# Kernel optimization log

Hardware: AMD Instinct MI355X
Metric: run time of the kernel (lower is better)

Reference implementation:

```python
import jax, jax.numpy as jnp
import numpy as np

N_NODES = 50000
N_EDGES = 800000
IN_DIM, HID, OUT_DIM = 128, 128, 64
BN_EPS = 1e-5


def setup_inputs() -> dict:
    key = jax.random.key(0)
    ks = jax.random.split(key, 16)
    x = jax.random.normal(ks[0], (N_NODES, IN_DIM), dtype=jnp.float32)
    edge_index = jax.random.randint(ks[1], (2, N_EDGES), 0, N_NODES, dtype=jnp.int64)
    s = 0.05
    params = {
        'Wl1': jax.random.normal(ks[2], (HID, IN_DIM), jnp.float32) * s,
        'Wr1': jax.random.normal(ks[3], (HID, IN_DIM), jnp.float32) * s,
        'b1': jnp.zeros((HID,), jnp.float32),
        'g1': jnp.ones((HID,), jnp.float32),
        'be1': jnp.zeros((HID,), jnp.float32),
        'Wl2': jax.random.normal(ks[4], (HID, HID), jnp.float32) * s,
        'Wr2': jax.random.normal(ks[5], (HID, HID), jnp.float32) * s,
        'b2': jnp.zeros((HID,), jnp.float32),
        'g2': jnp.ones((HID,), jnp.float32),
        'be2': jnp.zeros((HID,), jnp.float32),
        'Wl3': jax.random.normal(ks[6], (OUT_DIM, HID), jnp.float32) * s,
        'Wr3': jax.random.normal(ks[7], (OUT_DIM, HID), jnp.float32) * s,
        'b3': jnp.zeros((OUT_DIM,), jnp.float32),
    }
    return {'x': x, 'edge_index': edge_index, **params}


def _sage_conv(x, src, dst, Wl, Wr, b):
    # PyG SAGEConv (mean): out = lin_l(mean_{j in N(i)} x_j) + lin_r(x_i)
    msg = x[src]  # [E, d] gather
    agg = jax.ops.segment_sum(msg, dst, num_segments=N_NODES)
    cnt = jax.ops.segment_sum(jnp.ones((src.shape[0],), x.dtype), dst, num_segments=N_NODES)
    mean = agg / jnp.maximum(cnt, 1.0)[:, None]
    return mean @ Wl.T + x @ Wr.T + b


def _bn(h, gamma, beta):
    mu = jnp.mean(h, axis=0)
    var = jnp.var(h, axis=0)
    return (h - mu) * jax.lax.rsqrt(var + BN_EPS) * gamma + beta


def reference(x, edge_index, Wl1, Wr1, b1, g1, be1, Wl2, Wr2, b2, g2, be2, Wl3, Wr3, b3):
    src, dst = edge_index[0], edge_index[1]
    h = _sage_conv(x, src, dst, Wl1, Wr1, b1)
    h = jax.nn.relu(_bn(h, g1, be1))
    h = _sage_conv(h, src, dst, Wl2, Wr2, b2)
    h = jax.nn.relu(_bn(h, g2, be2))
    h = _sage_conv(h, src, dst, Wl3, Wr3, b3)
    return h
```

## Files before the change

### kernel.cpp

```cpp
#include <hip/hip_runtime.h>

#define N_NODES 50000
#define N_EDGES 800000
#define BN_EPS 1e-5f
#define NB 196
#define BCAP 5120
#define SCAT_BLOCKS 400
#define EPB 2000
#define GGRID 391

typedef __bf16 bf16x8 __attribute__((ext_vector_type(8)));
typedef float f32x4 __attribute__((ext_vector_type(4)));

static __device__ __forceinline__ unsigned short f2b(float f) {
    unsigned int u = __float_as_uint(f);
    return (unsigned short)((u + 0x7FFFu + ((u >> 16) & 1u)) >> 16);
}
static __device__ __forceinline__ float bl(unsigned int u) { return __uint_as_float(u << 16); }
static __device__ __forceinline__ float bh(unsigned int u) { return __uint_as_float(u & 0xFFFF0000u); }

static __device__ __forceinline__ void gload16(const void* g, void* l) {
    __builtin_amdgcn_global_load_lds(
        (const __attribute__((address_space(1))) unsigned int*)g,
        (__attribute__((address_space(3))) unsigned int*)l, 16, 0, 0);
}

__global__ void init_gcur(int* __restrict__ gcur) {
    int t = threadIdx.x;
    if (t < NB) gcur[t] = t * BCAP;
}

__global__ __launch_bounds__(256) void bucket_scatter(const int* __restrict__ ei,
                                                      int* __restrict__ gcur,
                                                      unsigned int* __restrict__ bdata) {
    __shared__ int hist[NB];
    __shared__ int lcur[NB];
    int t = threadIdx.x;
    if (t < NB) hist[t] = 0;
    __syncthreads();
    int e0 = blockIdx.x * EPB;
    for (int i = t; i < EPB; i += 256) {
        int d = ei[N_EDGES + e0 + i];
        atomicAdd(&hist[d >> 8], 1);
    }
    __syncthreads();
    if (t < NB) lcur[t] = atomicAdd(&gcur[t], hist[t]);
    __syncthreads();
    for (int i = t; i < EPB; i += 256) {
        int d = ei[N_EDGES + e0 + i];
        int s = ei[e0 + i];
        int b = d >> 8;
        int p = atomicAdd(&lcur[b], 1);
        if (p < (b + 1) * BCAP)
            bdata[p] = (unsigned int)s | ((unsigned int)(d & 255) << 16);
    }
}

__global__ __launch_bounds__(256) void scan_buckets(const int* __restrict__ gcur,
                                                    int* __restrict__ bbase,
                                                    int* __restrict__ row) {
    __shared__ int sm[256];
    int t = threadIdx.x;
    int v = 0;
    if (t < NB) {
        v = gcur[t] - t * BCAP;
        if (v > BCAP) v = BCAP;
    }
    sm[t] = v;
    __syncthreads();
    int x = v;
    for (int off = 1; off < 256; off <<= 1) {
        int y = (t >= off) ? sm[t - off] : 0;
        __syncthreads();
        x += y;
        sm[t] = x;
        __syncthreads();
    }
    if (t < NB) bbase[t] = x - v;
    if (t == 0) row[N_NODES] = N_EDGES;
}

__global__ __launch_bounds__(256) void bucket_fill(const unsigned int* __restrict__ bdata,
                                                   const int* __restrict__ gcur,
                                                   const int* __restrict__ bbase,
                                                   int* __restrict__ row,
                                                   int* __restrict__ csrc) {
    __shared__ unsigned int ent[BCAP];
    __shared__ int lcnt[256];
    __shared__ int sm[256];
    __shared__ int cur[256];
    int b = blockIdx.x;
    int t = threadIdx.x;
    int cnt = gcur[b] - b * BCAP;
    if (cnt > BCAP) cnt = BCAP;
    int base = bbase[b];
    for (int i = t; i < cnt; i += 256) ent[i] = bdata[b * BCAP + i];
    lcnt[t] = 0;
    __syncthreads();
    for (int i = t; i < cnt; i += 256) atomicAdd(&lcnt[(ent[i] >> 16) & 255], 1);
    __syncthreads();
    int v = lcnt[t];
    sm[t] = v;
    __syncthreads();
    int x = v;
    for (int off = 1; off < 256; off <<= 1) {
        int y = (t >= off) ? sm[t - off] : 0;
        __syncthreads();
        x += y;
        sm[t] = x;
        __syncthreads();
    }
    int pre = x - v;
    int node = b * 256 + t;
    if (node < N_NODES) row[node] = base + pre;
    cur[t] = base + pre;
    __syncthreads();
    for (int i = t; i < cnt; i += 256) {
        unsigned int e = ent[i];
        int p = atomicAdd(&cur[(e >> 16) & 255], 1);
        csrc[p] = (int)(e & 0xFFFFu);
    }
}

__global__ __launch_bounds__(256) void cast_x(const float* __restrict__ in,
                                              unsigned short* __restrict__ out) {
    int idx = blockIdx.x * 256 + threadIdx.x;
    if (idx >= N_NODES * 32) return;
    float4 v = ((const float4*)in)[idx];
    uint2 p;
    p.x = (unsigned int)f2b(v.x) | ((unsigned int)f2b(v.y) << 16);
    p.y = (unsigned int)f2b(v.z) | ((unsigned int)f2b(v.w) << 16);
    ((uint2*)out)[idx] = p;
}

__global__ void wpack(const float* __restrict__ Wl1, const float* __restrict__ Wr1,
                      const float* __restrict__ Wl2, const float* __restrict__ Wr2,
                      const float* __restrict__ Wl3, const float* __restrict__ Wr3,
                      unsigned short* __restrict__ wp) {
    int idx = blockIdx.x * 256 + threadIdx.x;
    if (idx >= 81920) return;
    const float *Wl, *Wr;
    int rel, base;
    if (idx < 32768)       { Wl = Wl1; Wr = Wr1; rel = idx;         base = 0; }
    else if (idx < 65536)  { Wl = Wl2; Wr = Wr2; rel = idx - 32768; base = 32768; }
    else                   { Wl = Wl3; Wr = Wr3; rel = idx - 65536; base = 65536; }
    int o = rel >> 8;
    int k = rel & 255;
    float v = (k < 128) ? Wl[o * 128 + k] : Wr[o * 128 + (k - 128)];
    int nfAll = o >> 4, lr = o & 15;
    int kc = k >> 5, ko = (k >> 3) & 3, kj = k & 7;
    int lane = ko * 16 + lr;
    wp[base + (((nfAll * 8 + kc) * 64 + lane) << 3) + kj] = f2b(v);
}

template <bool ACT>
__global__ __launch_bounds__(256) void agg_mean_bf16(const unsigned short* __restrict__ xin,
                                                     const int* __restrict__ row,
                                                     const int* __restrict__ csrc,
                                                     const float* __restrict__ scl,
                                                     const float* __restrict__ shf,
                                                     unsigned short* __restrict__ mean) {
    int half = threadIdx.x >> 5;
    int hl = threadIdx.x & 31;
    int node = blockIdx.x * 8 + half;
    if (node >= N_NODES) return;
    float4 sc{}, sh{};
    if (ACT) {
        sc = ((const float4*)scl)[hl];
        sh = ((const float4*)shf)[hl];
    }
    int r0 = row[node], r1 = row[node + 1];
    const uint2* x2 = (const uint2*)xin;
    float a0 = 0.f, a1 = 0.f, a2 = 0.f, a3 = 0.f;
    auto val = [&](float raw, float s, float h) {
        return ACT ? fmaxf(fmaf(raw, s, h), 0.f) : raw;
    };
    int j = r0;
    for (; j + 1 < r1; j += 2) {
        int s0 = csrc[j];
        int s1 = csrc[j + 1];
        uint2 v0 = x2[(size_t)s0 * 32 + hl];
        uint2 v1 = x2[(size_t)s1 * 32 + hl];
        a0 += val(bl(v0.x), sc.x, sh.x) + val(bl(v1.x), sc.x, sh.x);
        a1 += val(bh(v0.x), sc.y, sh.y) + val(bh(v1.x), sc.y, sh.y);
        a2 += val(bl(v0.y), sc.z, sh.z) + val(bl(v1.y), sc.z, sh.z);
        a3 += val(bh(v0.y), sc.w, sh.w) + val(bh(v1.y), sc.w, sh.w);
    }
    if (j < r1) {
        uint2 v = x2[(size_t)csrc[j] * 32 + hl];
        a0 += val(bl(v.x), sc.x, sh.x);
        a1 += val(bh(v.x), sc.y, sh.y);
        a2 += val(bl(v.y), sc.z, sh.z);
        a3 += val(bh(v.y), sc.w, sh.w);
    }
    int deg = r1 - r0;
    float inv = 1.0f / (float)(deg > 1 ? deg : 1);
    uint2 pk;
    pk.x = (unsigned int)f2b(a0 * inv) | ((unsigned int)f2b(a1 * inv) << 16);
    pk.y = (unsigned int)f2b(a2 * inv) | ((unsigned int)f2b(a3 * inv) << 16);
    ((uint2*)mean)[(size_t)node * 32 + hl] = pk;
}

template <int O, bool BF16OUT, bool STATS, bool ACTX>
__global__ __launch_bounds__(256, 1) void gemm_mfma(const unsigned short* __restrict__ Am,
                                                    const unsigned short* __restrict__ Ax,
                                                    const unsigned short* __restrict__ wp,
                                                    const float* __restrict__ bias,
                                                    const float* __restrict__ sclx,
                                                    const float* __restrict__ shfx,
                                                    unsigned short* __restrict__ hout,
                                                    float* __restrict__ fout,
                                                    float* __restrict__ cs,
                                                    float* __restrict__ cq) {
    constexpr int NFW = O / 64;
    __shared__ uint4 abuf[4096];
    char* lds = (char*)abuf;
    int t = threadIdx.x;
    int wv = t >> 6, l = t & 63;
    int lr = l & 15, ko = l >> 4;

    int t0 = blockIdx.x;
    int t1 = t0 + GGRID;

    uint4 wfr[NFW][8];
#pragma unroll
    for (int nf = 0; nf < NFW; ++nf)
#pragma unroll
        for (int kc = 0; kc < 8; ++kc)
            wfr[nf][kc] = *(const uint4*)(wp + (size_t)(((wv * NFW + nf) * 8 + kc) * 512) + l * 8);

    float sacc[NFW], qacc[NFW];
#pragma unroll
    for (int nf = 0; nf < NFW; ++nf) { sacc[nf] = 0.f; qacc[nf] = 0.f; }

    auto STAGE = [&](int buf, int tile) {
        int rbase = tile * 64;
        char* bdst = lds + buf * 32768;
#pragma unroll
        for (int i = 0; i < 8; ++i) {
            int sb = wv * 8 + i;
            int half = sb >> 4;
            int rloc = (sb & 15) * 4 + (l >> 4);
            int grow = rbase + rloc;
            if (grow >= N_NODES) grow = N_NODES - 1;
            int clog = (l & 15) ^ (rloc & 7);
            const unsigned short* src = half ? Ax : Am;
            gload16(src + (size_t)grow * 128 + clog * 8, bdst + sb * 1024);
        }
    };

    auto COMPUTE = [&](int buf, int tile) {
        const char* ab = lds + buf * 32768;
        f32x4 acc[4][NFW];
#pragma unroll
        for (int rt = 0; rt < 4; ++rt)
#pragma unroll
            for (int nf = 0; nf < NFW; ++nf) acc[rt][nf] = (f32x4){0.f, 0.f, 0.f, 0.f};

#pragma unroll
        for (int kc = 0; kc < 8; ++kc) {
            int clog = (kc & 3) * 4 + ko;
            float4 s0{}, s1{}, h0{}, h1{};
            if (ACTX && kc >= 4) {
                int f0 = clog * 8;
                s0 = *(const float4*)(sclx + f0);
                s1 = *(const float4*)(sclx + f0 + 4);
                h0 = *(const float4*)(shfx + f0);
                h1 = *(const float4*)(shfx + f0 + 4);
            }
#pragma unroll
            for (int rt = 0; rt < 4; ++rt) {
                int rloc = rt * 16 + lr;
                int cphys = clog ^ (rloc & 7);
                bf16x8 af = *(const bf16x8*)(ab + (kc >> 2) * 16384 + rloc * 256 + cphys * 16);
                if (ACTX && kc >= 4) {
                    uint4 u = *(uint4*)&af;
                    uint4 r;
                    float e0 = fmaxf(fmaf(bl(u.x), s0.x, h0.x), 0.f);
                    float e1 = fmaxf(fmaf(bh(u.x), s0.y, h0.y), 0.f);
                    float e2 = fmaxf(fmaf(bl(u.y), s0.z, h0.z), 0.f);
                    float e3 = fmaxf(fmaf(bh(u.y), s0.w, h0.w), 0.f);
                    float e4 = fmaxf(fmaf(bl(u.z), s1.x, h1.x), 0.f);
                    float e5 = fmaxf(fmaf(bh(u.z), s1.y, h1.y), 0.f);
                    float e6 = fmaxf(fmaf(bl(u.w), s1.z, h1.z), 0.f);
                    float e7 = fmaxf(fmaf(bh(u.w), s1.w, h1.w), 0.f);
                    r.x = (unsigned int)f2b(e0) | ((unsigned int)f2b(e1) << 16);
                    r.y = (unsigned int)f2b(e2) | ((unsigned int)f2b(e3) << 16);
                    r.z = (unsigned int)f2b(e4) | ((unsigned int)f2b(e5) << 16);
                    r.w = (unsigned int)f2b(e6) | ((unsigned int)f2b(e7) << 16);
                    af = *(bf16x8*)&r;
                }
#pragma unroll
                for (int nf = 0; nf < NFW; ++nf) {
                    bf16x8 wf = *(bf16x8*)&wfr[nf][kc];
                    acc[rt][nf] = __builtin_amdgcn_mfma_f32_16x16x32_bf16(af, wf, acc[rt][nf], 0, 0, 0);
                }
            }
        }

        int rbase = tile * 64;
#pragma unroll
        for (int rt = 0; rt < 4; ++rt) {
            int orow0 = rbase + rt * 16 + ko * 4;
#pragma unroll
            for (int nf = 0; nf < NFW; ++nf) {
                int col = (wv * NFW + nf) * 16 + lr;
                float bs = bias[col];
#pragma unroll
                for (int j = 0; j < 4; ++j) {
                    int r = orow0 + j;
                    if (r < N_NODES) {
                        float v = acc[rt][nf][j] + bs;
                        if (BF16OUT) hout[(size_t)r * 128 + col] = f2b(v);
                        else         fout[(size_t)r * 64 + col] = v;
                        if (STATS) { sacc[nf] += v; qacc[nf] += v * v; }
                    }
                }
            }
        }
    };

    STAGE(0, t0);
    __syncthreads();
    STAGE(1, t1);
    COMPUTE(0, t0);
    __syncthreads();
    COMPUTE(1, t1);

    if (STATS) {
#pragma unroll
        for (int nf = 0; nf < NFW; ++nf) {
            float s = sacc[nf], q = qacc[nf];
            s += __shfl_xor(s, 16);
            s += __shfl_xor(s, 32);
            q += __shfl_xor(q, 16);
            q += __shfl_xor(q, 32);
            if (ko == 0) {
                int col = (wv * NFW + nf) * 16 + lr;
                atomicAdd(&cs[col], s);
                atomicAdd(&cq[col], q);
            }
        }
    }
}

__global__ void bn_prep(const float* __restrict__ cs, const float* __restrict__ cq,
                        const float* __restrict__ g, const float* __restrict__ be,
                        float* __restrict__ scale, float* __restrict__ shift) {
    int f = threadIdx.x;
    float mu = cs[f] * (1.0f / N_NODES);
    float var = cq[f] * (1.0f / N_NODES) - mu * mu;
    float sc = g[f] * rsqrtf(var + BN_EPS);
    scale[f] = sc;
    shift[f] = be[f] - mu * sc;
}

extern "C" void kernel_launch(void* const* d_in, const int* in_sizes, int n_in,
                              void* d_out, int out_size, void* d_ws, size_t ws_size,
                              hipStream_t stream) {
    const float* x   = (const float*)d_in[0];
    const int*   ei  = (const int*)d_in[1];
    const float* Wl1 = (const float*)d_in[2];
    const float* Wr1 = (const float*)d_in[3];
    const float* b1  = (const float*)d_in[4];
    const float* g1  = (const float*)d_in[5];
    const float* be1 = (const float*)d_in[6];
    const float* Wl2 = (const float*)d_in[7];
    const float* Wr2 = (const float*)d_in[8];
    const float* b2  = (const float*)d_in[9];
    const float* g2  = (const float*)d_in[10];
    const float* be2 = (const float*)d_in[11];
    const float* Wl3 = (const float*)d_in[12];
    const float* Wr3 = (const float*)d_in[13];
    const float* b3  = (const float*)d_in[14];
    float* out = (float*)d_out;

    char* p = (char*)d_ws;
    size_t off = 0;
    auto alloc = [&](size_t bytes) {
        char* r = p + off;
        off = (off + bytes + 255) & ~(size_t)255;
        return r;
    };
    int*            gcur  = (int*)alloc((size_t)NB * 4);
    int*            bbase = (int*)alloc((size_t)NB * 4);
    unsigned int*   bdata = (unsigned int*)alloc((size_t)NB * BCAP * 4);
    int*            row   = (int*)alloc((size_t)(N_NODES + 1) * 4);
    int*            csrc  = (int*)alloc((size_t)N_EDGES * 4);
    unsigned short* xb    = (unsigned short*)alloc((size_t)N_NODES * 128 * 2);
    unsigned short* mn    = (unsigned short*)alloc((size_t)N_NODES * 128 * 2);
    unsigned short* h1    = (unsigned short*)alloc((size_t)N_NODES * 128 * 2);
    unsigned short* h2    = (unsigned short*)alloc((size_t)N_NODES * 128 * 2);
    unsigned short* wpb   = (unsigned short*)alloc((size_t)81920 * 2);
    float*          cs    = (float*)alloc(256 * 4);
    float*          cq    = cs + 128;
    float*          scl1  = (float*)alloc(128 * 4);
    float*          shf1  = (float*)alloc(128 * 4);
    float*          scl2  = (float*)alloc(128 * 4);
    float*          shf2  = (float*)alloc(128 * 4);
    (void)ws_size; (void)n_in; (void)in_sizes; (void)out_size;

    unsigned short* wp1 = wpb;
    unsigned short* wp2 = wpb + 32768;
    unsigned short* wp3 = wpb + 65536;

    const int NBLK8 = (N_NODES + 7) / 8;
    const int CBLK  = (N_NODES * 32 + 255) / 256;

    cast_x<<<CBLK, 256, 0, stream>>>(x, xb);
    wpack<<<320, 256, 0, stream>>>(Wl1, Wr1, Wl2, Wr2, Wl3, Wr3, wpb);
    init_gcur<<<1, 256, 0, stream>>>(gcur);
    bucket_scatter<<<SCAT_BLOCKS, 256, 0, stream>>>(ei, gcur, bdata);
    scan_buckets<<<1, 256, 0, stream>>>(gcur, bbase, row);
    bucket_fill<<<NB, 256, 0, stream>>>(bdata, gcur, bbase, row, csrc);

    agg_mean_bf16<false><<<NBLK8, 256, 0, stream>>>(xb, row, csrc, nullptr, nullptr, mn);
    hipMemsetAsync(cs, 0, 256 * 4, stream);
    gemm_mfma<128, true, true, false><<<GGRID, 256, 0, stream>>>(
        mn, xb, wp1, b1, nullptr, nullptr, h1, nullptr, cs, cq);
    bn_prep<<<1, 128, 0, stream>>>(cs, cq, g1, be1, scl1, shf1);

    agg_mean_bf16<true><<<NBLK8, 256, 0, stream>>>(h1, row, csrc, scl1, shf1, mn);
    hipMemsetAsync(cs, 0, 256 * 4, stream);
    gemm_mfma<128, true, true, true><<<GGRID, 256, 0, stream>>>(
        mn, h1, wp2, b2, scl1, shf1, h2, nullptr, cs, cq);
    bn_prep<<<1, 128, 0, stream>>>(cs, cq, g2, be2, scl2, shf2);

    agg_mean_bf16<true><<<NBLK8, 256, 0, stream>>>(h2, row, csrc, scl2, shf2, mn);
    gemm_mfma<64, false, false, true><<<GGRID, 256, 0, stream>>>(
        mn, h2, wp3, b3, scl2, shf2, nullptr, out, nullptr, nullptr);
}
```

Baseline: 229.1 us.

## Shrink GEMM tiles to 32 rows per block and raise occupancy

The node-feature GEMM now processes one 32-row tile per block over 1563 blocks, instead of two 64-row tiles per block over 391 blocks with one block per CU. It drops the occupancy-1 launch bound and cuts LDS from 64 KB to 16 KB so several blocks can share a CU and hide load latency. It also widens the XOR swizzle to 16 and starts the tile load before the weight-fragment load. In exchange, each block reloads its weight fragments into registers, so weight traffic roughly quadruples. The number of BN-statistics atomics per column also rises with the block count.

```diff
diff --git a/kernel.cpp b/kernel.cpp
--- a/kernel.cpp
+++ b/kernel.cpp
@@ -7,7 +7,7 @@
 #define BCAP 5120
 #define SCAT_BLOCKS 400
 #define EPB 2000
-#define GGRID 391
+#define GRB 1563
 
 typedef __bf16 bf16x8 __attribute__((ext_vector_type(8)));
 typedef float f32x4 __attribute__((ext_vector_type(4)));
@@ -202,25 +202,35 @@
 }
 
 template <int O, bool BF16OUT, bool STATS, bool ACTX>
-__global__ __launch_bounds__(256, 1) void gemm_mfma(const unsigned short* __restrict__ Am,
-                                                    const unsigned short* __restrict__ Ax,
-                                                    const unsigned short* __restrict__ wp,
-                                                    const float* __restrict__ bias,
-                                                    const float* __restrict__ sclx,
-                                                    const float* __restrict__ shfx,
-                                                    unsigned short* __restrict__ hout,
-                                                    float* __restrict__ fout,
-                                                    float* __restrict__ cs,
-                                                    float* __restrict__ cq) {
+__global__ __launch_bounds__(256) void gemm_mfma(const unsigned short* __restrict__ Am,
+                                                 const unsigned short* __restrict__ Ax,
+                                                 const unsigned short* __restrict__ wp,
+                                                 const float* __restrict__ bias,
+                                                 const float* __restrict__ sclx,
+                                                 const float* __restrict__ shfx,
+                                                 unsigned short* __restrict__ hout,
+                                                 float* __restrict__ fout,
+                                                 float* __restrict__ cs,
+                                                 float* __restrict__ cq) {
     constexpr int NFW = O / 64;
-    __shared__ uint4 abuf[4096];
+    __shared__ uint4 abuf[1024];
     char* lds = (char*)abuf;
     int t = threadIdx.x;
     int wv = t >> 6, l = t & 63;
     int lr = l & 15, ko = l >> 4;
-
-    int t0 = blockIdx.x;
-    int t1 = t0 + GGRID;
+    int rbase = blockIdx.x * 32;
+
+#pragma unroll
+    for (int i = 0; i < 4; ++i) {
+        int sb = wv * 4 + i;
+        int half = sb >> 3;
+        int rloc = (sb & 7) * 4 + (l >> 4);
+        int grow = rbase + rloc;
+        if (grow >= N_NODES) grow = N_NODES - 1;
+        int clog = (l & 15) ^ (rloc & 15);
+        const unsigned short* src = half ? Ax : Am;
+        gload16(src + (size_t)grow * 128 + clog * 8, lds + sb * 1024);
+    }
 
     uint4 wfr[NFW][8];
 #pragma unroll
@@ -229,116 +239,84 @@
         for (int kc = 0; kc < 8; ++kc)
             wfr[nf][kc] = *(const uint4*)(wp + (size_t)(((wv * NFW + nf) * 8 + kc) * 512) + l * 8);
 
-    float sacc[NFW], qacc[NFW];
-#pragma unroll
-    for (int nf = 0; nf < NFW; ++nf) { sacc[nf] = 0.f; qacc[nf] = 0.f; }
-
-    auto STAGE = [&](int buf, int tile) {
-        int rbase = tile * 64;
-        char* bdst = lds + buf * 32768;
-#pragma unroll
-        for (int i = 0; i < 8; ++i) {
-            int sb = wv * 8 + i;
-            int half = sb >> 4;
-            int rloc = (sb & 15) * 4 + (l >> 4);
-            int grow = rbase + rloc;
-            if (grow >= N_NODES) grow = N_NODES - 1;
-            int clog = (l & 15) ^ (rloc & 7);
-            const unsigned short* src = half ? Ax : Am;
-            gload16(src + (size_t)grow * 128 + clog * 8, bdst + sb * 1024);
+    __syncthreads();
+
+    f32x4 acc[2][NFW];
+#pragma unroll
+    for (int rt = 0; rt < 2; ++rt)
+#pragma unroll
+        for (int nf = 0; nf < NFW; ++nf) acc[rt][nf] = (f32x4){0.f, 0.f, 0.f, 0.f};
+
+#pragma unroll
+    for (int kc = 0; kc < 8; ++kc) {
+        int clog = (kc & 3) * 4 + ko;
+        float4 s0{}, s1{}, h0{}, h1{};
+        if (ACTX && kc >= 4) {
+            int f0 = clog * 8;
+            s0 = *(const float4*)(sclx + f0);
+            s1 = *(const float4*)(sclx + f0 + 4);
+            h0 = *(const float4*)(shfx + f0);
+            h1 = *(const float4*)(shfx + f0 + 4);
         }
-    };
-
-    auto COMPUTE = [&](int buf, int tile) {
-        const char* ab = lds + buf * 32768;
-        f32x4 acc[4][NFW];
-#pragma unroll
-        for (int rt = 0; rt < 4; ++rt)
-#pragma unroll
-            for (int nf = 0; nf < NFW; ++nf) acc[rt][nf] = (f32x4){0.f, 0.f, 0.f, 0.f};
-
-#pragma unroll
-        for (int kc = 0; kc < 8; ++kc) {
-            int clog = (kc & 3) * 4 + ko;
-            float4 s0{}, s1{}, h0{}, h1{};
+#pragma unroll
+        for (int rt = 0; rt < 2; ++rt) {
+            int rloc = rt * 16 + lr;
+            int cphys = clog ^ (rloc & 15);
+            bf16x8 af = *(const bf16x8*)(lds + (kc >> 2) * 8192 + rloc * 256 + cphys * 16);
             if (ACTX && kc >= 4) {
-                int f0 = clog * 8;
-                s0 = *(const float4*)(sclx + f0);
-                s1 = *(const float4*)(sclx + f0 + 4);
-                h0 = *(const float4*)(shfx + f0);
-                h1 = *(const float4*)(shfx + f0 + 4);
+                uint4 u = *(uint4*)&af;
+                uint4 r;
+                float e0 = fmaxf(fmaf(bl(u.x), s0.x, h0.x), 0.f);
+                float e1 = fmaxf(fmaf(bh(u.x), s0.y, h0.y), 0.f);
+                float e2 = fmaxf(fmaf(bl(u.y), s0.z, h0.z), 0.f);
+                float e3 = fmaxf(fmaf(bh(u.y), s0.w, h0.w), 0.f);
+                float e4 = fmaxf(fmaf(bl(u.z), s1.x, h1.x), 0.f);
+                float e5 = fmaxf(fmaf(bh(u.z), s1.y, h1.y), 0.f);
+                float e6 = fmaxf(fmaf(bl(u.w), s1.z, h1.z), 0.f);
+                float e7 = fmaxf(fmaf(bh(u.w), s1.w, h1.w), 0.f);
+                r.x = (unsigned int)f2b(e0) | ((unsigned int)f2b(e1) << 16);
+                r.y = (unsigned int)f2b(e2) | ((unsigned int)f2b(e3) << 16);
+                r.z = (unsigned int)f2b(e4) | ((unsigned int)f2b(e5) << 16);
+                r.w = (unsigned int)f2b(e6) | ((unsigned int)f2b(e7) << 16);
+                af = *(bf16x8*)&r;
             }
 #pragma unroll
-            for (int rt = 0; rt < 4; ++rt) {
-                int rloc = rt * 16 + lr;
-                int cphys = clog ^ (rloc & 7);
-                bf16x8 af = *(const bf16x8*)(ab + (kc >> 2) * 16384 + rloc * 256 + cphys * 16);
-                if (ACTX && kc >= 4) {
-                    uint4 u = *(uint4*)&af;
-                    uint4 r;
-                    float e0 = fmaxf(fmaf(bl(u.x), s0.x, h0.x), 0.f);
-                    float e1 = fmaxf(fmaf(bh(u.x), s0.y, h0.y), 0.f);
-                    float e2 = fmaxf(fmaf(bl(u.y), s0.z, h0.z), 0.f);
-                    float e3 = fmaxf(fmaf(bh(u.y), s0.w, h0.w), 0.f);
-                    float e4 = fmaxf(fmaf(bl(u.z), s1.x, h1.x), 0.f);
-                    float e5 = fmaxf(fmaf(bh(u.z), s1.y, h1.y), 0.f);
-                    float e6 = fmaxf(fmaf(bl(u.w), s1.z, h1.z), 0.f);
-                    float e7 = fmaxf(fmaf(bh(u.w), s1.w, h1.w), 0.f);
-                    r.x = (unsigned int)f2b(e0) | ((unsigned int)f2b(e1) << 16);
-                    r.y = (unsigned int)f2b(e2) | ((unsigned int)f2b(e3) << 16);
-                    r.z = (unsigned int)f2b(e4) | ((unsigned int)f2b(e5) << 16);
-                    r.w = (unsigned int)f2b(e6) | ((unsigned int)f2b(e7) << 16);
-                    af = *(bf16x8*)&r;
-                }
-#pragma unroll
-                for (int nf = 0; nf < NFW; ++nf) {
-                    bf16x8 wf = *(bf16x8*)&wfr[nf][kc];
-                    acc[rt][nf] = __builtin_amdgcn_mfma_f32_16x16x32_bf16(af, wf, acc[rt][nf], 0, 0, 0);
+            for (int nf = 0; nf < NFW; ++nf) {
+                bf16x8 wf = *(bf16x8*)&wfr[nf][kc];
+                acc[rt][nf] = __builtin_amdgcn_mfma_f32_16x16x32_bf16(af, wf, acc[rt][nf], 0, 0, 0);
+            }
+        }
+    }
+
+#pragma unroll
+    for (int rt = 0; rt < 2; ++rt) {
+        int orow0 = rbase + rt * 16 + ko * 4;
+#pragma unroll
+        for (int nf = 0; nf < NFW; ++nf) {
+            int col = (wv * NFW + nf) * 16 + lr;
+            float bs = bias[col];
+            float s = 0.f, q = 0.f;
+#pragma unroll
+            for (int j = 0; j < 4; ++j) {
+                int r = orow0 + j;
+                if (r < N_NODES) {
+                    float v = acc[rt][nf][j] + bs;
+                    if (BF16OUT) hout[(size_t)r * 128 + col] = f2b(v);
+                    else         fout[(size_t)r * 64 + col] = v;
+                    s += v;
+                    q += v * v;
                 }
             }
-        }
-
-        int rbase = tile * 64;
-#pragma unroll
-        for (int rt = 0; rt < 4; ++rt) {
-            int orow0 = rbase + rt * 16 + ko * 4;
-#pragma unroll
-            for (int nf = 0; nf < NFW; ++nf) {
-                int col = (wv * NFW + nf) * 16 + lr;
-                float bs = bias[col];
-#pragma unroll
-                for (int j = 0; j < 4; ++j) {
-                    int r = orow0 + j;
-                    if (r < N_NODES) {
-                        float v = acc[rt][nf][j] + bs;
-                        if (BF16OUT) hout[(size_t)r * 128 + col] = f2b(v);
-                        else         fout[(size_t)r * 64 + col] = v;
-                        if (STATS) { sacc[nf] += v; qacc[nf] += v * v; }
-                    }
+            if (STATS) {
+                s += __shfl_xor(s, 16);
+                s += __shfl_xor(s, 32);
+                q += __shfl_xor(q, 16);
+                q += __shfl_xor(q, 32);
+                if (ko == 0) {
+                    int col2 = (wv * NFW + nf) * 16 + lr;
+                    atomicAdd(&cs[col2], s);
+                    atomicAdd(&cq[col2], q);
                 }
-            }
-        }
-    };
-
-    STAGE(0, t0);
-    __syncthreads();
-    STAGE(1, t1);
-    COMPUTE(0, t0);
-    __syncthreads();
-    COMPUTE(1, t1);
-
-    if (STATS) {
-#pragma unroll
-        for (int nf = 0; nf < NFW; ++nf) {
-            float s = sacc[nf], q = qacc[nf];
-            s += __shfl_xor(s, 16);
-            s += __shfl_xor(s, 32);
-            q += __shfl_xor(q, 16);
-            q += __shfl_xor(q, 32);
-            if (ko == 0) {
-                int col = (wv * NFW + nf) * 16 + lr;
-                atomicAdd(&cs[col], s);
-                atomicAdd(&cq[col], q);
             }
         }
     }
@@ -416,17 +394,17 @@
 
     agg_mean_bf16<false><<<NBLK8, 256, 0, stream>>>(xb, row, csrc, nullptr, nullptr, mn);
     hipMemsetAsync(cs, 0, 256 * 4, stream);
-    gemm_mfma<128, true, true, false><<<GGRID, 256, 0, stream>>>(
+    gemm_mfma<128, true, true, false><<<GRB, 256, 0, stream>>>(
         mn, xb, wp1, b1, nullptr, nullptr, h1, nullptr, cs, cq);
     bn_prep<<<1, 128, 0, stream>>>(cs, cq, g1, be1, scl1, shf1);
 
     agg_mean_bf16<true><<<NBLK8, 256, 0, stream>>>(h1, row, csrc, scl1, shf1, mn);
     hipMemsetAsync(cs, 0, 256 * 4, stream);
-    gemm_mfma<128, true, true, true><<<GGRID, 256, 0, stream>>>(
+    gemm_mfma<128, true, true, true><<<GRB, 256, 0, stream>>>(
         mn, h1, wp2, b2, scl1, shf1, h2, nullptr, cs, cq);
     bn_prep<<<1, 128, 0, stream>>>(cs, cq, g2, be2, scl2, shf2);
 
     agg_mean_bf16<true><<<NBLK8, 256, 0, stream>>>(h2, row, csrc, scl2, shf2, mn);
-    gemm_mfma<64, false, false, true><<<GGRID, 256, 0, stream>>>(
+    gemm_mfma<64, false, false, true><<<GRB, 256, 0, stream>>>(
         mn, h2, wp3, b3, scl2, shf2, nullptr, out, nullptr, nullptr);
 }
```

After: 337.7 us. +47.4%, slower.
